# Optimization experiments

Measured on AMD Instinct MI355X. Metric: run time of the kernel, lower is better.

The kernel has to match this reference:

```python
import jax, jax.numpy as jnp
from jax import lax
import numpy as np

B, CIN, HID, H, W = 4, 64, 64, 64, 64
K, N, D = 3, 9, 256
INC = CIN + HID          # input_dim + hidden_dim = 128
OUTC = 4 * HID           # 4 LSTM gates = 256


def setup_inputs() -> dict:
    key = jax.random.key(0)
    ks = jax.random.split(key, 13)
    f = jax.random.normal
    return {
        "input_tensor": f(ks[0], (B, CIN, H, W), jnp.float32),
        "h_cur": f(ks[1], (B, HID, H, W), jnp.float32),
        "c_cur": f(ks[2], (B, HID, H, W), jnp.float32),
        "meta_info": f(ks[3], (B, D), jnp.float32),
        "meta_info_offset": f(ks[4], (B, 1, H, W), jnp.float32),
        "w1_w": f(ks[5], (INC * D, D), jnp.float32) / 16.0,
        "w1_b": f(ks[6], (INC * D,), jnp.float32) * 0.02,
        "w2_w": f(ks[7], (OUTC * K * K, D), jnp.float32) / 16.0,
        "w2_b": f(ks[8], (OUTC * K * K,), jnp.float32) * 0.02,
        "bl_w": f(ks[9], (OUTC, D), jnp.float32) / 16.0,
        "bl_b": f(ks[10], (OUTC,), jnp.float32) * 0.02,
        "pconv_w": f(ks[11], (2 * K * K, 1, 3, 3), jnp.float32) * 0.05,
        "pconv_b": f(ks[12], (2 * K * K,), jnp.float32) * 0.05,
    }


def reference(input_tensor, h_cur, c_cur, meta_info, meta_info_offset,
              w1_w, w1_b, w2_w, w2_b, bl_w, bl_b, pconv_w, pconv_b):
    b = input_tensor.shape[0]
    # --- hypernetwork: per-sample conv weights (b, out, in, k*k) and biases ---
    wm = (meta_info @ w1_w.T + w1_b).reshape(b, INC, D)
    wm = (jnp.einsum('bcd,od->bco', wm, w2_w) + w2_b).reshape(b, INC, OUTC, K, K)
    wm = wm.transpose(0, 2, 1, 3, 4).reshape(b, OUTC, INC, N)      # (b,o,c,9)
    bm = (meta_info @ bl_w.T + bl_b)[:, :, None, None]             # (b,o,1,1)
    # --- concat + zero pad (ZeroPad2d(1)) ---
    x = jnp.concatenate([input_tensor, h_cur], axis=1)             # (b,INC,H,W)
    x = jnp.pad(x, ((0, 0), (0, 0), (1, 1), (1, 1)))               # (b,INC,H+2,W+2)
    Hp, Wp = H + 2, W + 2
    # --- offset field from p_conv (3x3, pad 1) ---
    offset = lax.conv_general_dilated(
        meta_info_offset, pconv_w, (1, 1), ((1, 1), (1, 1)),
        dimension_numbers=('NCHW', 'OIHW', 'NCHW')) + pconv_b[None, :, None, None]
    # --- sampling positions p = p_0 + p_n + offset ; channel layout [x*N, y*N] ---
    r = jnp.arange(-(K // 2), K // 2 + 1, dtype=jnp.float32)
    pn_x = jnp.repeat(r, K)                                        # meshgrid 'ij' rows
    pn_y = jnp.tile(r, K)
    p0_x = jnp.broadcast_to(jnp.arange(1, H + 1, dtype=jnp.float32)[:, None], (H, W))
    p0_y = jnp.broadcast_to(jnp.arange(1, W + 1, dtype=jnp.float32)[None, :], (H, W))
    p = jnp.concatenate([
        p0_x[None, None] + pn_x[None, :, None, None],
        p0_y[None, None] + pn_y[None, :, None, None],
    ], axis=1) + offset                                            # (b,2N,H,W)
    p = p.transpose(0, 2, 3, 1)                                    # (b,H,W,2N)

    def clampxy(q):
        return jnp.concatenate([jnp.clip(q[..., :N], 0, Hp - 1),
                                jnp.clip(q[..., N:], 0, Wp - 1)], axis=-1)

    q_floor = jnp.floor(lax.stop_gradient(p))
    q_lt = clampxy(q_floor)
    q_rb = clampxy(q_floor + 1)
    q_lb = jnp.concatenate([q_lt[..., :N], q_rb[..., N:]], axis=-1)
    q_rt = jnp.concatenate([q_rb[..., :N], q_lt[..., N:]], axis=-1)
    p = clampxy(p)
    # bilinear corner weights (exact torch expressions, grads flow through p)
    g_lt = (1 + (q_lt[..., :N] - p[..., :N])) * (1 + (q_lt[..., N:] - p[..., N:]))
    g_rb = (1 - (q_rb[..., :N] - p[..., :N])) * (1 - (q_rb[..., N:] - p[..., N:]))
    g_lb = (1 + (q_lb[..., :N] - p[..., :N])) * (1 - (q_lb[..., N:] - p[..., N:]))
    g_rt = (1 - (q_rt[..., :N] - p[..., :N])) * (1 + (q_rt[..., N:] - p[..., N:]))

    x_flat = x.reshape(b, INC, Hp * Wp)

    def sample(q):
        idx = (q[..., :N] * Wp + q[..., N:]).astype(jnp.int32).reshape(b, 1, -1)
        return jnp.take_along_axis(x_flat, idx, axis=2).reshape(b, INC, H, W, N)

    x_off = (g_lt[:, None] * sample(q_lt) + g_rb[:, None] * sample(q_rb)
             + g_lb[:, None] * sample(q_lb) + g_rt[:, None] * sample(q_rt))
    # dynamic grouped conv (groups=b, stride=k on the k-tiled map) == per-sample
    # contraction over (in_channel, kernel tap)
    combined = jnp.einsum('bchwn,bocn->bohw', x_off, wm) + bm      # (b,4*HID,H,W)
    cc_i, cc_f, cc_o, cc_g = jnp.split(combined, 4, axis=1)
    i = jax.nn.sigmoid(cc_i)
    f = jax.nn.sigmoid(cc_f)
    o = jax.nn.sigmoid(cc_o)
    g = jnp.tanh(cc_g)
    c_next = f * c_cur + i * g
    h_next = o * jnp.tanh(c_next)
    return (h_next, c_next)
```

## Files before the change

kernel.cpp:

```cpp
#include <hip/hip_runtime.h>
#include <math.h>

#define Bn    4
#define HIDc  64
#define INCc  128
#define OUTCc 256
#define Dd    256
#define NT    9
#define HWn   4096
#define NC    18

typedef _Float16 f16;
typedef unsigned short u16;
typedef __attribute__((ext_vector_type(8))) _Float16 h8;
typedef __attribute__((ext_vector_type(4))) float f4;

#define WM1_OFF 0
#define BM_OFF  (Bn*INCc*Dd)
#define F16_BYTE_OFF ((size_t)(BM_OFF + Bn*OUTCc) * 4)
#define TX_ELEMS ((size_t)Bn*HWn*INCc)

__device__ __forceinline__ float sigf(float x) { return 1.f / (1.f + __expf(-x)); }
__device__ __forceinline__ float tanhfast(float x) {
    float a = fabsf(x);
    float e = __expf(2.f * a);
    float t = 1.f - 2.f / (e + 1.f);
    return copysignf(t, x);
}

__global__ void __launch_bounds__(256)
k_tr(const float* __restrict__ xin, const float* __restrict__ hcur,
     f16* __restrict__ tx)
{
    int b = blockIdx.x >> 6, h = blockIdx.x & 63;
    int t = threadIdx.x;
    int w = t & 63, oq = t >> 6;
    const float* xb = xin  + ((size_t)b * HIDc) * HWn + h * 64;
    const float* hb = hcur + ((size_t)b * HIDc) * HWn + h * 64;
    f16* dst = tx + ((size_t)(b * HWn + h * 64 + w)) * INCc;
#pragma unroll
    for (int s = 0; s < 4; s++) {
        int c0 = (oq + s * 4) * 8;
        h8 v;
#pragma unroll
        for (int i = 0; i < 8; i++) {
            int ci = c0 + i;
            float f = (ci < HIDc) ? xb[(size_t)ci * HWn + w]
                                  : hb[(size_t)(ci - HIDc) * HWn + w];
            v[i] = (f16)f;
        }
        *(h8*)(dst + c0) = v;
    }
}

__global__ void __launch_bounds__(256)
k_hyper(const float* __restrict__ meta, const float* __restrict__ w1w,
        const float* __restrict__ w1b, const float* __restrict__ blw,
        const float* __restrict__ blb, float* __restrict__ ws)
{
    __shared__ __align__(16) float sm[Bn * Dd];
    int t = threadIdx.x;
    for (int i = t; i < Bn * Dd; i += 256) sm[i] = meta[i];
    __syncthreads();

    int lane = t & 63, wvv = t >> 6;
    int rl = lane >> 4, dl = lane & 15;
    int rbase = blockIdx.x * 64 + wvv * 16;

#pragma unroll
    for (int g = 0; g < 4; g++) {
        int r = rbase + g * 4 + rl;
        bool isbl = (r >= INCc * Dd);
        const float* row = isbl ? (blw + (size_t)(r - INCc * Dd) * Dd)
                                : (w1w + (size_t)r * Dd);
        float a0 = 0.f, a1 = 0.f, a2 = 0.f, a3 = 0.f;
#pragma unroll
        for (int it = 0; it < 4; it++) {
            int d = it * 64 + dl * 4;
            float4 wv = *(const float4*)(row + d);
            float4 m0 = *(const float4*)&sm[0 * Dd + d];
            float4 m1 = *(const float4*)&sm[1 * Dd + d];
            float4 m2 = *(const float4*)&sm[2 * Dd + d];
            float4 m3 = *(const float4*)&sm[3 * Dd + d];
            a0 += wv.x*m0.x + wv.y*m0.y + wv.z*m0.z + wv.w*m0.w;
            a1 += wv.x*m1.x + wv.y*m1.y + wv.z*m1.z + wv.w*m1.w;
            a2 += wv.x*m2.x + wv.y*m2.y + wv.z*m2.z + wv.w*m2.w;
            a3 += wv.x*m3.x + wv.y*m3.y + wv.z*m3.z + wv.w*m3.w;
        }
#pragma unroll
        for (int mk = 1; mk <= 8; mk <<= 1) {
            a0 += __shfl_xor(a0, mk); a1 += __shfl_xor(a1, mk);
            a2 += __shfl_xor(a2, mk); a3 += __shfl_xor(a3, mk);
        }
        if (dl == 0) {
            if (isbl) {
                int rb = r - INCc * Dd;
                float bb = blb[rb];
                ws[BM_OFF + 0*OUTCc + rb] = a0 + bb;
                ws[BM_OFF + 1*OUTCc + rb] = a1 + bb;
                ws[BM_OFF + 2*OUTCc + rb] = a2 + bb;
                ws[BM_OFF + 3*OUTCc + rb] = a3 + bb;
            } else {
                float bb = w1b[r];
                ws[WM1_OFF + 0*INCc*Dd + r] = a0 + bb;
                ws[WM1_OFF + 1*INCc*Dd + r] = a1 + bb;
                ws[WM1_OFF + 2*INCc*Dd + r] = a2 + bb;
                ws[WM1_OFF + 3*INCc*Dd + r] = a3 + bb;
            }
        }
    }
}

__global__ void __launch_bounds__(256)
k_w2(const float* __restrict__ w2w, const float* __restrict__ w2b,
     const float* __restrict__ ws, f16* __restrict__ wh)
{
    int bid = blockIdx.x;
    int b   = bid / 144;
    int r   = bid % 144;
    int mt  = r / 36, nt = r % 36;
    int c0  = mt * 32, j0 = nt * 64;

    __shared__ __align__(16) float At[32][34];
    __shared__ __align__(16) float Bt[32][68];

    const float* A = ws + WM1_OFF + (size_t)b * INCc * Dd;
    int t   = threadIdx.x;
    int lrA = t >> 3, lfA = t & 7;
    int lrB = t >> 2, lfB = t & 3;
    int ty  = t >> 4, tx = t & 15;

    float acc[2][4];
#pragma unroll
    for (int i = 0; i < 2; i++)
#pragma unroll
        for (int q = 0; q < 4; q++) acc[i][q] = 0.f;

    for (int dk = 0; dk < Dd; dk += 32) {
        __syncthreads();
        {
            float4 av = *(const float4*)(A + (size_t)(c0 + lrA) * Dd + dk + lfA * 4);
            At[lfA*4+0][lrA] = av.x; At[lfA*4+1][lrA] = av.y;
            At[lfA*4+2][lrA] = av.z; At[lfA*4+3][lrA] = av.w;
        }
#pragma unroll
        for (int s = 0; s < 2; s++) {
            int f = lfB + s * 4;
            float4 bv = *(const float4*)(w2w + (size_t)(j0 + lrB) * Dd + dk + f * 4);
            Bt[f*4+0][lrB] = bv.x; Bt[f*4+1][lrB] = bv.y;
            Bt[f*4+2][lrB] = bv.z; Bt[f*4+3][lrB] = bv.w;
        }
        __syncthreads();
#pragma unroll 4
        for (int d = 0; d < 32; d++) {
            float2 a2 = *(const float2*)&At[d][ty * 2];
            float4 b4 = *(const float4*)&Bt[d][tx * 4];
            acc[0][0] += a2.x*b4.x; acc[0][1] += a2.x*b4.y;
            acc[0][2] += a2.x*b4.z; acc[0][3] += a2.x*b4.w;
            acc[1][0] += a2.y*b4.x; acc[1][1] += a2.y*b4.y;
            acc[1][2] += a2.y*b4.z; acc[1][3] += a2.y*b4.w;
        }
    }

#pragma unroll
    for (int i = 0; i < 2; i++) {
        int c = c0 + ty * 2 + i;
#pragma unroll
        for (int q = 0; q < 4; q++) {
            int j = j0 + tx * 4 + q;
            int o = j / 9, n = j - o * 9;
            float v = acc[i][q] + w2b[j];
            int k  = n * 128 + c;
            int kc = k >> 6, kk = k & 63;
            int rr = ((o & 63) << 2) | (o >> 6);
            wh[((size_t)(b * NC + kc) * 256 + rr) * 64 + kk] = (f16)v;
        }
    }
}

__global__ void __launch_bounds__(256)
k_main(const f16* __restrict__ tx, const float* __restrict__ ccur,
       const float* __restrict__ moff, const float* __restrict__ pw,
       const float* __restrict__ pb, const float* __restrict__ ws,
       const f16* __restrict__ wh, float* __restrict__ out)
{
    int bid  = blockIdx.x;
    int xcd  = bid & 7;
    int b    = xcd >> 1;
    int tile = ((bid >> 3) << 1) + (xcd & 1);
    int h    = tile >> 1;
    int w0   = (tile & 1) * 32;

    __shared__ __align__(16) int   sIdx[NT][4][32];
    __shared__ __align__(16) float sWgt[NT][4][32];
    __shared__ __align__(16) f16   Xs[2][32][64];
    __shared__ float bmS[OUTCc];

    int t = threadIdx.x;
    bmS[t] = ws[BM_OFF + b * OUTCc + t];

    {
        int px   = t & 31;
        int nh   = t >> 5;
        int wpos = w0 + px;
        for (int n = nh; n < NT; n += 8) {
            float ox = pb[n], oy = pb[NT + n];
#pragma unroll
            for (int ii = 0; ii < 3; ii++) {
#pragma unroll
                for (int jj = 0; jj < 3; jj++) {
                    int rr = h - 1 + ii, cc = wpos - 1 + jj;
                    float m = (rr >= 0 && rr < 64 && cc >= 0 && cc < 64)
                              ? moff[(size_t)b * HWn + rr * 64 + cc] : 0.f;
                    ox = fmaf(pw[(size_t)n * 9 + ii * 3 + jj], m, ox);
                    oy = fmaf(pw[(size_t)(NT + n) * 9 + ii * 3 + jj], m, oy);
                }
            }
            float pr = (float)(h + (n / 3)) + ox;
            float pc = (float)(wpos + (n % 3)) + oy;
            float fr = floorf(pr), fc = floorf(pc);
            float ltr = fminf(fmaxf(fr, 0.f), 65.f);
            float ltc = fminf(fmaxf(fc, 0.f), 65.f);
            float rbr = fminf(fmaxf(fr + 1.f, 0.f), 65.f);
            float rbc = fminf(fmaxf(fc + 1.f, 0.f), 65.f);
            float cpr = fminf(fmaxf(pr, 0.f), 65.f);
            float cpc = fminf(fmaxf(pc, 0.f), 65.f);
            float ar = 1.f + ltr - cpr, br = 1.f - rbr + cpr;
            float ac = 1.f + ltc - cpc, bc = 1.f - rbc + cpc;
            int ir0 = (int)ltr, ic0 = (int)ltc, ir1 = (int)rbr, ic1 = (int)rbc;
            int   rr4[4] = {ir0, ir1, ir0, ir1};
            int   cc4[4] = {ic0, ic1, ic1, ic0};
            float gg4[4] = {ar * ac, br * bc, ar * bc, br * ac};
#pragma unroll
            for (int jj = 0; jj < 4; jj++) {
                bool inb = (rr4[jj] >= 1) && (rr4[jj] <= 64) &&
                           (cc4[jj] >= 1) && (cc4[jj] <= 64);
                sIdx[n][jj][px] = inb ? ((rr4[jj] - 1) * 64 + (cc4[jj] - 1)) : 0;
                sWgt[n][jj][px] = inb ? gg4[jj] : 0.f;
            }
        }
    }
    __syncthreads();

    int px   = t & 31;
    int oct  = t >> 5;
    int lane = t & 63;
    int wv   = t >> 6;
    int col  = lane & 15;
    int quad = lane >> 4;

    const f16* txb = tx + (size_t)b * HWn * INCc;

    auto sample_chunk = [&](int KC, int BUF) {
        int n_ = KC >> 1;
        int coff = ((KC & 1) << 6) + (oct << 3);
        const f16* p0 = txb + (size_t)sIdx[n_][0][px] * INCc + coff;
        const f16* p1 = txb + (size_t)sIdx[n_][1][px] * INCc + coff;
        const f16* p2 = txb + (size_t)sIdx[n_][2][px] * INCc + coff;
        const f16* p3 = txb + (size_t)sIdx[n_][3][px] * INCc + coff;
        float g0 = sWgt[n_][0][px], g1 = sWgt[n_][1][px],
              g2 = sWgt[n_][2][px], g3 = sWgt[n_][3][px];
        h8 v0 = *(const h8*)p0;
        h8 v1 = *(const h8*)p1;
        h8 v2 = *(const h8*)p2;
        h8 v3 = *(const h8*)p3;
        h8 res;
#pragma unroll
        for (int i = 0; i < 8; i++) {
            float v = g0 * (float)v0[i] + g1 * (float)v1[i]
                    + g2 * (float)v2[i] + g3 * (float)v3[i];
            res[i] = (f16)v;
        }
        *(h8*)&Xs[BUF][px][(oct ^ (px & 7)) << 3] = res;
    };

    f4 acc[4][2];
#pragma unroll
    for (int oi = 0; oi < 4; oi++)
#pragma unroll
        for (int pj = 0; pj < 2; pj++) acc[oi][pj] = (f4){0.f, 0.f, 0.f, 0.f};

    const f16* whb = wh + (size_t)b * NC * 256 * 64;

    sample_chunk(0, 0);
    __syncthreads();

    for (int kc = 0; kc < NC; kc++) {
        int cur = kc & 1;
        h8 Af[4][2];
#pragma unroll
        for (int oi = 0; oi < 4; oi++)
#pragma unroll
            for (int ks = 0; ks < 2; ks++)
                Af[oi][ks] = *(const h8*)(whb +
                    ((size_t)kc * 256 + wv * 64 + oi * 16 + col) * 64 + ks * 32 + quad * 8);
        h8 Bf[2][2];
#pragma unroll
        for (int pj = 0; pj < 2; pj++)
#pragma unroll
            for (int ks = 0; ks < 2; ks++) {
                int pxx = pj * 16 + col;
                int g   = ks * 4 + quad;
                Bf[pj][ks] = *(const h8*)&Xs[cur][pxx][(g ^ (pxx & 7)) << 3];
            }
        if (kc < NC - 1) sample_chunk(kc + 1, cur ^ 1);
#pragma unroll
        for (int oi = 0; oi < 4; oi++)
#pragma unroll
            for (int pj = 0; pj < 2; pj++) {
                acc[oi][pj] = __builtin_amdgcn_mfma_f32_16x16x32_f16(Af[oi][0], Bf[pj][0], acc[oi][pj], 0, 0, 0);
                acc[oi][pj] = __builtin_amdgcn_mfma_f32_16x16x32_f16(Af[oi][1], Bf[pj][1], acc[oi][pj], 0, 0, 0);
            }
        __syncthreads();
    }

#pragma unroll
    for (int oi = 0; oi < 4; oi++) {
        int ch = wv * 16 + oi * 4 + quad;
#pragma unroll
        for (int pj = 0; pj < 2; pj++) {
            int wpos = w0 + pj * 16 + col;
            f4 a = acc[oi][pj];
            float ci  = a[0] + bmS[ch];
            float cf  = a[1] + bmS[64 + ch];
            float co  = a[2] + bmS[128 + ch];
            float cgv = a[3] + bmS[192 + ch];
            float ig  = sigf(ci);
            float fg  = sigf(cf);
            float og_ = sigf(co);
            float gg  = tanhfast(cgv);
            size_t idx = (((size_t)(b * HIDc + ch)) * 64 + h) * 64 + wpos;
            float cp = ccur[idx];
            float cn = fg * cp + ig * gg;
            out[idx] = og_ * tanhfast(cn);
            out[(size_t)Bn * HIDc * HWn + idx] = cn;
        }
    }
}

extern "C" void kernel_launch(void* const* d_in, const int* in_sizes, int n_in,
                              void* d_out, int out_size, void* d_ws, size_t ws_size,
                              hipStream_t stream)
{
    const float* xin  = (const float*)d_in[0];
    const float* hcur = (const float*)d_in[1];
    const float* ccur = (const float*)d_in[2];
    const float* meta = (const float*)d_in[3];
    const float* moff = (const float*)d_in[4];
    const float* w1w  = (const float*)d_in[5];
    const float* w1b  = (const float*)d_in[6];
    const float* w2w  = (const float*)d_in[7];
    const float* w2b  = (const float*)d_in[8];
    const float* blw  = (const float*)d_in[9];
    const float* blb  = (const float*)d_in[10];
    const float* pw   = (const float*)d_in[11];
    const float* pb   = (const float*)d_in[12];
    float* out = (float*)d_out;
    float* ws  = (float*)d_ws;
    f16*   tx  = (f16*)((char*)d_ws + F16_BYTE_OFF);
    f16*   wh  = tx + TX_ELEMS;

    hipLaunchKernelGGL(k_tr,    dim3(256), dim3(256), 0, stream, xin, hcur, tx);
    hipLaunchKernelGGL(k_hyper, dim3(516), dim3(256), 0, stream,
                       meta, w1w, w1b, blw, blb, ws);
    hipLaunchKernelGGL(k_w2,    dim3(576), dim3(256), 0, stream, w2w, w2b, ws, wh);
    hipLaunchKernelGGL(k_main,  dim3(512), dim3(256), 0, stream,
                       tx, ccur, moff, pw, pb, ws, wh, out);
}
```

Baseline: 184.1 us.

## Use split-f16 MFMA for hypernet GEMM and stage weights via LDS DMA

The second hypernetwork GEMM switches from scalar fp32 FMAs to MFMA. Its activation operand is split into hi/lo f16 halves to keep precision, while w2 is rounded to f16. The main kernel now processes a full 64-pixel row per 512-thread block. It stages the per-chunk weight tile into LDS with global_load_lds in a swizzled layout instead of each wave loading weights from global memory. The aim is to cut FP32 ALU time in k_w2 and reduce redundant global weight traffic in k_main. The cost is fewer blocks, more LDS per block, and an extra barrier per chunk because sampling is no longer double-buffered.

```diff
diff --git a/kernel.cpp b/kernel.cpp
--- a/kernel.cpp
+++ b/kernel.cpp
@@ -12,13 +12,16 @@
 
 typedef _Float16 f16;
 typedef unsigned short u16;
+typedef unsigned int u32;
 typedef __attribute__((ext_vector_type(8))) _Float16 h8;
 typedef __attribute__((ext_vector_type(4))) float f4;
 
-#define WM1_OFF 0
-#define BM_OFF  (Bn*INCc*Dd)
-#define F16_BYTE_OFF ((size_t)(BM_OFF + Bn*OUTCc) * 4)
-#define TX_ELEMS ((size_t)Bn*HWn*INCc)
+#define BM_OFF   0
+#define F16_BYTE 4096
+#define TX_F   ((size_t)0)
+#define WH_F   ((size_t)2097152)
+#define M1H_F  ((size_t)3276800)
+#define M1L_F  ((size_t)3407872)
 
 __device__ __forceinline__ float sigf(float x) { return 1.f / (1.f + __expf(-x)); }
 __device__ __forceinline__ float tanhfast(float x) {
@@ -56,7 +59,8 @@
 __global__ void __launch_bounds__(256)
 k_hyper(const float* __restrict__ meta, const float* __restrict__ w1w,
         const float* __restrict__ w1b, const float* __restrict__ blw,
-        const float* __restrict__ blb, float* __restrict__ ws)
+        const float* __restrict__ blb, float* __restrict__ bm,
+        f16* __restrict__ m1h, f16* __restrict__ m1l)
 {
     __shared__ __align__(16) float sm[Bn * Dd];
     int t = threadIdx.x;
@@ -96,16 +100,20 @@
             if (isbl) {
                 int rb = r - INCc * Dd;
                 float bb = blb[rb];
-                ws[BM_OFF + 0*OUTCc + rb] = a0 + bb;
-                ws[BM_OFF + 1*OUTCc + rb] = a1 + bb;
-                ws[BM_OFF + 2*OUTCc + rb] = a2 + bb;
-                ws[BM_OFF + 3*OUTCc + rb] = a3 + bb;
+                bm[0*OUTCc + rb] = a0 + bb;
+                bm[1*OUTCc + rb] = a1 + bb;
+                bm[2*OUTCc + rb] = a2 + bb;
+                bm[3*OUTCc + rb] = a3 + bb;
             } else {
                 float bb = w1b[r];
-                ws[WM1_OFF + 0*INCc*Dd + r] = a0 + bb;
-                ws[WM1_OFF + 1*INCc*Dd + r] = a1 + bb;
-                ws[WM1_OFF + 2*INCc*Dd + r] = a2 + bb;
-                ws[WM1_OFF + 3*INCc*Dd + r] = a3 + bb;
+                float v[4] = {a0 + bb, a1 + bb, a2 + bb, a3 + bb};
+#pragma unroll
+                for (int bi = 0; bi < 4; bi++) {
+                    f16 hi = (f16)v[bi];
+                    f16 lo = (f16)(v[bi] - (float)hi);
+                    m1h[(size_t)bi * 32768 + r] = hi;
+                    m1l[(size_t)bi * 32768 + r] = lo;
+                }
             }
         }
     }
@@ -113,103 +121,110 @@
 
 __global__ void __launch_bounds__(256)
 k_w2(const float* __restrict__ w2w, const float* __restrict__ w2b,
-     const float* __restrict__ ws, f16* __restrict__ wh)
+     const f16* __restrict__ m1h, const f16* __restrict__ m1l,
+     f16* __restrict__ wh)
 {
     int bid = blockIdx.x;
     int b   = bid / 144;
-    int r   = bid % 144;
-    int mt  = r / 36, nt = r % 36;
-    int c0  = mt * 32, j0 = nt * 64;
-
-    __shared__ __align__(16) float At[32][34];
-    __shared__ __align__(16) float Bt[32][68];
-
-    const float* A = ws + WM1_OFF + (size_t)b * INCc * Dd;
-    int t   = threadIdx.x;
-    int lrA = t >> 3, lfA = t & 7;
-    int lrB = t >> 2, lfB = t & 3;
-    int ty  = t >> 4, tx = t & 15;
-
-    float acc[2][4];
-#pragma unroll
-    for (int i = 0; i < 2; i++)
-#pragma unroll
-        for (int q = 0; q < 4; q++) acc[i][q] = 0.f;
-
-    for (int dk = 0; dk < Dd; dk += 32) {
-        __syncthreads();
-        {
-            float4 av = *(const float4*)(A + (size_t)(c0 + lrA) * Dd + dk + lfA * 4);
-            At[lfA*4+0][lrA] = av.x; At[lfA*4+1][lrA] = av.y;
-            At[lfA*4+2][lrA] = av.z; At[lfA*4+3][lrA] = av.w;
-        }
-#pragma unroll
-        for (int s = 0; s < 2; s++) {
-            int f = lfB + s * 4;
-            float4 bv = *(const float4*)(w2w + (size_t)(j0 + lrB) * Dd + dk + f * 4);
-            Bt[f*4+0][lrB] = bv.x; Bt[f*4+1][lrB] = bv.y;
-            Bt[f*4+2][lrB] = bv.z; Bt[f*4+3][lrB] = bv.w;
-        }
-        __syncthreads();
-#pragma unroll 4
-        for (int d = 0; d < 32; d++) {
-            float2 a2 = *(const float2*)&At[d][ty * 2];
-            float4 b4 = *(const float4*)&Bt[d][tx * 4];
-            acc[0][0] += a2.x*b4.x; acc[0][1] += a2.x*b4.y;
-            acc[0][2] += a2.x*b4.z; acc[0][3] += a2.x*b4.w;
-            acc[1][0] += a2.y*b4.x; acc[1][1] += a2.y*b4.y;
-            acc[1][2] += a2.y*b4.z; acc[1][3] += a2.y*b4.w;
-        }
-    }
-
-#pragma unroll
-    for (int i = 0; i < 2; i++) {
-        int c = c0 + ty * 2 + i;
-#pragma unroll
-        for (int q = 0; q < 4; q++) {
-            int j = j0 + tx * 4 + q;
-            int o = j / 9, n = j - o * 9;
-            float v = acc[i][q] + w2b[j];
+    int rem = bid % 144;
+    int c0  = (rem / 36) * 32;
+    int j0  = (rem % 36) * 64;
+
+    __shared__ __align__(16) f16 Ah[32][256];
+    __shared__ __align__(16) f16 Al[32][256];
+    __shared__ __align__(16) f16 Bh[64][256];
+
+    int t = threadIdx.x;
+    {
+        int row = t >> 3, seg = t & 7;
+        const f16* sh = m1h + (size_t)b * 32768 + (size_t)(c0 + row) * 256 + seg * 32;
+        const f16* sl = m1l + (size_t)b * 32768 + (size_t)(c0 + row) * 256 + seg * 32;
+#pragma unroll
+        for (int i = 0; i < 4; i++) {
+            int gsl = ((seg * 4 + i) ^ (row & 7)) * 8;
+            *(h8*)&Ah[row][gsl] = *(const h8*)(sh + i * 8);
+            *(h8*)&Al[row][gsl] = *(const h8*)(sl + i * 8);
+        }
+        int row2 = t >> 2, seg2 = t & 3;
+        const float* sb = w2w + (size_t)(j0 + row2) * 256 + seg2 * 64;
+#pragma unroll
+        for (int i = 0; i < 8; i++) {
+            float4 x0 = *(const float4*)(sb + i * 8);
+            float4 x1 = *(const float4*)(sb + i * 8 + 4);
+            h8 v = {(f16)x0.x, (f16)x0.y, (f16)x0.z, (f16)x0.w,
+                    (f16)x1.x, (f16)x1.y, (f16)x1.z, (f16)x1.w};
+            *(h8*)&Bh[row2][((seg2 * 8 + i) ^ (row2 & 7)) * 8] = v;
+        }
+    }
+    __syncthreads();
+
+    int lane = t & 63, jw = t >> 6;
+    int col = lane & 15, quad = lane >> 4;
+
+    f4 acc[2];
+    acc[0] = (f4){0.f, 0.f, 0.f, 0.f};
+    acc[1] = (f4){0.f, 0.f, 0.f, 0.f};
+#pragma unroll
+    for (int ks = 0; ks < 8; ks++) {
+        int gsl = ((ks * 4 + quad) ^ (col & 7)) * 8;
+        h8 Bf = *(const h8*)&Bh[jw * 16 + col][gsl];
+#pragma unroll
+        for (int cf = 0; cf < 2; cf++) {
+            h8 Ahf = *(const h8*)&Ah[cf * 16 + col][gsl];
+            h8 Alf = *(const h8*)&Al[cf * 16 + col][gsl];
+            acc[cf] = __builtin_amdgcn_mfma_f32_16x16x32_f16(Ahf, Bf, acc[cf], 0, 0, 0);
+            acc[cf] = __builtin_amdgcn_mfma_f32_16x16x32_f16(Alf, Bf, acc[cf], 0, 0, 0);
+        }
+    }
+
+    int j = j0 + jw * 16 + col;
+    int o = j / 9, n = j - o * 9;
+    float bias = w2b[j];
+    int rr = ((o & 63) << 2) | (o >> 6);
+    f16* whb = wh + (size_t)b * (NC * 16384);
+#pragma unroll
+    for (int cf = 0; cf < 2; cf++)
+#pragma unroll
+        for (int rg = 0; rg < 4; rg++) {
+            int c  = c0 + cf * 16 + quad * 4 + rg;
             int k  = n * 128 + c;
             int kc = k >> 6, kk = k & 63;
-            int rr = ((o & 63) << 2) | (o >> 6);
-            wh[((size_t)(b * NC + kc) * 256 + rr) * 64 + kk] = (f16)v;
-        }
-    }
-}
-
-__global__ void __launch_bounds__(256)
+            int slot = (kk >> 3) ^ (rr & 7);
+            whb[((size_t)kc * 256 + rr) * 64 + slot * 8 + (kk & 7)] =
+                (f16)(acc[cf][rg] + bias);
+        }
+}
+
+__global__ void __launch_bounds__(512)
 k_main(const f16* __restrict__ tx, const float* __restrict__ ccur,
        const float* __restrict__ moff, const float* __restrict__ pw,
-       const float* __restrict__ pb, const float* __restrict__ ws,
+       const float* __restrict__ pb, const float* __restrict__ bm,
        const f16* __restrict__ wh, float* __restrict__ out)
 {
-    int bid  = blockIdx.x;
-    int xcd  = bid & 7;
-    int b    = xcd >> 1;
-    int tile = ((bid >> 3) << 1) + (xcd & 1);
-    int h    = tile >> 1;
-    int w0   = (tile & 1) * 32;
-
-    __shared__ __align__(16) int   sIdx[NT][4][32];
-    __shared__ __align__(16) float sWgt[NT][4][32];
-    __shared__ __align__(16) f16   Xs[2][32][64];
+    int bid = blockIdx.x;
+    int xcd = bid & 7;
+    int b   = xcd >> 1;
+    int h   = ((bid >> 3) << 1) | (xcd & 1);
+
+    __shared__ u16   sIdx[NT][4][64];
+    __shared__ float sWgt[NT][4][64];
+    __shared__ __align__(16) f16 Wb[256 * 64];
+    __shared__ __align__(16) f16 Xs[64][64];
     __shared__ float bmS[OUTCc];
 
     int t = threadIdx.x;
-    bmS[t] = ws[BM_OFF + b * OUTCc + t];
+    if (t < 256) bmS[t] = bm[b * OUTCc + t];
 
     {
-        int px   = t & 31;
-        int nh   = t >> 5;
-        int wpos = w0 + px;
+        int px = t & 63;
+        int nh = t >> 6;
         for (int n = nh; n < NT; n += 8) {
             float ox = pb[n], oy = pb[NT + n];
 #pragma unroll
             for (int ii = 0; ii < 3; ii++) {
 #pragma unroll
                 for (int jj = 0; jj < 3; jj++) {
-                    int rr = h - 1 + ii, cc = wpos - 1 + jj;
+                    int rr = h - 1 + ii, cc = px - 1 + jj;
                     float m = (rr >= 0 && rr < 64 && cc >= 0 && cc < 64)
                               ? moff[(size_t)b * HWn + rr * 64 + cc] : 0.f;
                     ox = fmaf(pw[(size_t)n * 9 + ii * 3 + jj], m, ox);
@@ -217,7 +232,7 @@
                 }
             }
             float pr = (float)(h + (n / 3)) + ox;
-            float pc = (float)(wpos + (n % 3)) + oy;
+            float pc = (float)(px + (n % 3)) + oy;
             float fr = floorf(pr), fc = floorf(pc);
             float ltr = fminf(fmaxf(fr, 0.f), 65.f);
             float ltc = fminf(fmaxf(fc, 0.f), 65.f);
@@ -235,75 +250,88 @@
             for (int jj = 0; jj < 4; jj++) {
                 bool inb = (rr4[jj] >= 1) && (rr4[jj] <= 64) &&
                            (cc4[jj] >= 1) && (cc4[jj] <= 64);
-                sIdx[n][jj][px] = inb ? ((rr4[jj] - 1) * 64 + (cc4[jj] - 1)) : 0;
+                sIdx[n][jj][px] = (u16)(inb ? ((rr4[jj] - 1) * 64 + (cc4[jj] - 1)) : 0);
                 sWgt[n][jj][px] = inb ? gg4[jj] : 0.f;
             }
         }
     }
     __syncthreads();
 
-    int px   = t & 31;
-    int oct  = t >> 5;
-    int lane = t & 63;
-    int wv   = t >> 6;
-    int col  = lane & 15;
-    int quad = lane >> 4;
+    int lane  = t & 63;
+    int wv    = t >> 6;
+    int col   = lane & 15, quad = lane >> 4;
+    int ow    = wv & 3;
+    int ph    = wv >> 2;
+    int sp_px = t >> 3;
+    int sp_oc = t & 7;
 
     const f16* txb = tx + (size_t)b * HWn * INCc;
-
-    auto sample_chunk = [&](int KC, int BUF) {
+    const f16* whb = wh + (size_t)b * (NC * 16384);
+
+    auto sample = [&](int KC) {
         int n_ = KC >> 1;
-        int coff = ((KC & 1) << 6) + (oct << 3);
-        const f16* p0 = txb + (size_t)sIdx[n_][0][px] * INCc + coff;
-        const f16* p1 = txb + (size_t)sIdx[n_][1][px] * INCc + coff;
-        const f16* p2 = txb + (size_t)sIdx[n_][2][px] * INCc + coff;
-        const f16* p3 = txb + (size_t)sIdx[n_][3][px] * INCc + coff;
-        float g0 = sWgt[n_][0][px], g1 = sWgt[n_][1][px],
-              g2 = sWgt[n_][2][px], g3 = sWgt[n_][3][px];
+        int co = ((KC & 1) << 6) + sp_oc * 8;
+        const f16* p0 = txb + (size_t)sIdx[n_][0][sp_px] * INCc + co;
+        const f16* p1 = txb + (size_t)sIdx[n_][1][sp_px] * INCc + co;
+        const f16* p2 = txb + (size_t)sIdx[n_][2][sp_px] * INCc + co;
+        const f16* p3 = txb + (size_t)sIdx[n_][3][sp_px] * INCc + co;
+        float g0 = sWgt[n_][0][sp_px], g1 = sWgt[n_][1][sp_px];
+        float g2 = sWgt[n_][2][sp_px], g3 = sWgt[n_][3][sp_px];
         h8 v0 = *(const h8*)p0;
         h8 v1 = *(const h8*)p1;
         h8 v2 = *(const h8*)p2;
         h8 v3 = *(const h8*)p3;
         h8 res;
 #pragma unroll
-        for (int i = 0; i < 8; i++) {
-            float v = g0 * (float)v0[i] + g1 * (float)v1[i]
-                    + g2 * (float)v2[i] + g3 * (float)v3[i];
-            res[i] = (f16)v;
-        }
-        *(h8*)&Xs[BUF][px][(oct ^ (px & 7)) << 3] = res;
+        for (int i = 0; i < 8; i++)
+            res[i] = (f16)(g0 * (float)v0[i] + g1 * (float)v1[i]
+                         + g2 * (float)v2[i] + g3 * (float)v3[i]);
+        *(h8*)&Xs[sp_px][(sp_oc ^ (sp_px & 7)) * 8] = res;
     };
 
+    auto dmaW = [&](int KC) {
+        const f16* src = whb + (size_t)KC * 16384;
+#pragma unroll
+        for (int i = 0; i < 4; i++) {
+            int seg = i * 8 + wv;
+            const f16* g = src + seg * 512 + lane * 8;
+            f16* l = &Wb[seg * 512];
+            __builtin_amdgcn_global_load_lds(
+                (const __attribute__((address_space(1))) u32*)g,
+                (__attribute__((address_space(3))) u32*)l, 16, 0, 0);
+        }
+    };
+
     f4 acc[4][2];
 #pragma unroll
     for (int oi = 0; oi < 4; oi++)
 #pragma unroll
         for (int pj = 0; pj < 2; pj++) acc[oi][pj] = (f4){0.f, 0.f, 0.f, 0.f};
 
-    const f16* whb = wh + (size_t)b * NC * 256 * 64;
-
-    sample_chunk(0, 0);
+    dmaW(0);
+    sample(0);
     __syncthreads();
 
     for (int kc = 0; kc < NC; kc++) {
-        int cur = kc & 1;
-        h8 Af[4][2];
+        h8 Af[4][2], Bf[2][2];
 #pragma unroll
         for (int oi = 0; oi < 4; oi++)
 #pragma unroll
-            for (int ks = 0; ks < 2; ks++)
-                Af[oi][ks] = *(const h8*)(whb +
-                    ((size_t)kc * 256 + wv * 64 + oi * 16 + col) * 64 + ks * 32 + quad * 8);
-        h8 Bf[2][2];
+            for (int ks = 0; ks < 2; ks++) {
+                int rr   = ow * 64 + oi * 16 + col;
+                int slot = (ks * 4 + quad) ^ (col & 7);
+                Af[oi][ks] = *(const h8*)&Wb[rr * 64 + slot * 8];
+            }
 #pragma unroll
         for (int pj = 0; pj < 2; pj++)
 #pragma unroll
             for (int ks = 0; ks < 2; ks++) {
-                int pxx = pj * 16 + col;
-                int g   = ks * 4 + quad;
-                Bf[pj][ks] = *(const h8*)&Xs[cur][pxx][(g ^ (pxx & 7)) << 3];
-            }
-        if (kc < NC - 1) sample_chunk(kc + 1, cur ^ 1);
+                int px   = ph * 32 + pj * 16 + col;
+                int slot = (ks * 4 + quad) ^ (px & 7);
+                Bf[pj][ks] = *(const h8*)&Xs[px][slot * 8];
+            }
+        __syncthreads();
+        if (kc < NC - 1) { dmaW(kc + 1); sample(kc + 1); }
 #pragma unroll
         for (int oi = 0; oi < 4; oi++)
 #pragma unroll
@@ -316,10 +344,10 @@
 
 #pragma unroll
     for (int oi = 0; oi < 4; oi++) {
-        int ch = wv * 16 + oi * 4 + quad;
+        int ch = ow * 16 + oi * 4 + quad;
 #pragma unroll
         for (int pj = 0; pj < 2; pj++) {
-            int wpos = w0 + pj * 16 + col;
+            int wpos = ph * 32 + pj * 16 + col;
             f4 a = acc[oi][pj];
             float ci  = a[0] + bmS[ch];
             float cf  = a[1] + bmS[64 + ch];
@@ -356,14 +384,18 @@
     const float* pw   = (const float*)d_in[11];
     const float* pb   = (const float*)d_in[12];
     float* out = (float*)d_out;
-    float* ws  = (float*)d_ws;
-    f16*   tx  = (f16*)((char*)d_ws + F16_BYTE_OFF);
-    f16*   wh  = tx + TX_ELEMS;
+    float* bm  = (float*)d_ws;
+    f16* f16b  = (f16*)((char*)d_ws + F16_BYTE);
+    f16* tx  = f16b + TX_F;
+    f16* wh  = f16b + WH_F;
+    f16* m1h = f16b + M1H_F;
+    f16* m1l = f16b + M1L_F;
 
     hipLaunchKernelGGL(k_tr,    dim3(256), dim3(256), 0, stream, xin, hcur, tx);
     hipLaunchKernelGGL(k_hyper, dim3(516), dim3(256), 0, stream,
-                       meta, w1w, w1b, blw, blb, ws);
-    hipLaunchKernelGGL(k_w2,    dim3(576), dim3(256), 0, stream, w2w, w2b, ws, wh);
-    hipLaunchKernelGGL(k_main,  dim3(512), dim3(256), 0, stream,
-                       tx, ccur, moff, pw, pb, ws, wh, out);
-}
+                       meta, w1w, w1b, blw, blb, bm, m1h, m1l);
+    hipLaunchKernelGGL(k_w2,    dim3(576), dim3(256), 0, stream,
+                       w2w, w2b, m1h, m1l, wh);
+    hipLaunchKernelGGL(k_main,  dim3(256), dim3(512), 0, stream,
+                       tx, ccur, moff, pw, pb, bm, wh, out);
+}
```

Result: faster. 152.1 us (-17.4%).
